# Kernel tuning notes

Measured on AMD Instinct MI355X. Metric: run time of the kernel, lower is better.

Reference implementation:

```python
import jax, jax.numpy as jnp
import numpy as np

EPS = 1e-6

def _l2norm(x):
    # torch F.normalize(dim=1): x / max(||x||_2, eps), norm over channel axis 1
    n = jnp.sqrt(jnp.sum(x * x, axis=1, keepdims=True))
    return x / jnp.maximum(n, EPS)

def setup_inputs() -> dict:
    key = jax.random.key(0)
    ks = jax.random.split(key, 8)
    B, C, Cenc, dk, dv, H, W = 2, 320, 326, 64, 64, 64, 64
    return {
        "x": jax.random.normal(ks[0], (B, C, H, W), jnp.float32),
        "x_enc": jax.random.normal(ks[1], (B, Cenc, H, W), jnp.float32),
        "Wq": jax.random.normal(ks[2], (dk, Cenc), jnp.float32) * 0.05,
        "bq": jnp.zeros((dk,), jnp.float32),
        "Wk": jax.random.normal(ks[3], (dk, Cenc), jnp.float32) * 0.05,
        "bk": jnp.zeros((dk,), jnp.float32),
        "Wv": jax.random.normal(ks[4], (dv, C), jnp.float32) * 0.05,
        "bv": jnp.zeros((dv,), jnp.float32),
    }

def reference(x, x_enc, Wq, bq, Wk, bk, Wv, bv):
    B, C, H, Wd = x.shape
    L = H * Wd
    xe = x_enc.reshape(B, x_enc.shape[1], L)   # [B, Cenc, L]
    xf = x.reshape(B, C, L)                    # [B, C, L]
    # 1x1 conv projections == channel matmuls
    Q = jnp.einsum('oc,bcl->bol', Wq, xe) + bq[None, :, None]  # [B, dk, L]
    K = jnp.einsum('oc,bcl->bol', Wk, xe) + bk[None, :, None]  # [B, dk, L]
    V = jnp.einsum('oc,bcl->bol', Wv, xf) + bv[None, :, None]  # [B, dv, L]
    # cosine (L2-normalized) attention
    Qn = _l2norm(Q)
    Kn = _l2norm(K)
    A = jax.nn.softmax(jnp.einsum('bqi,bqj->bij', Qn, Kn), axis=-1)  # [B, L, L]
    R = jnp.einsum('bij,bvj->bvi', A, V)       # [B, dv, L]
    return R.reshape(B, V.shape[1], H, Wd)
```

## Files before the change

### kernel.cpp

```cpp
#include <hip/hip_runtime.h>


#define L_DIM 4096
#define KPAD 384
#define NSPLIT 8

typedef __attribute__((ext_vector_type(8))) short bf16x8;
typedef __attribute__((ext_vector_type(4))) float f32x4;

__device__ __forceinline__ unsigned short f2bf(float f) {
    unsigned u = __float_as_uint(f);
    u += 0x7fffu + ((u >> 16) & 1u);
    return (unsigned short)(u >> 16);
}

__global__ __launch_bounds__(256) void prep_kernel(
    const float* __restrict__ x, const float* __restrict__ xe,
    const float* __restrict__ Wq, const float* __restrict__ Wk,
    const float* __restrict__ Wv,
    unsigned short* __restrict__ xt_x, unsigned short* __restrict__ xt_xe,
    unsigned short* __restrict__ wbf)
{
    const int z = blockIdx.z;
    if (z == 4) {
        const int bid = blockIdx.y * 64 + blockIdx.x;
        const int idx = bid * 256 + threadIdx.x;
        if (idx >= 3 * 64 * KPAD) return;
        const int t = idx / (64 * KPAD);
        const int rem = idx - t * 64 * KPAD;
        const int d = rem / KPAD, c = rem - d * KPAD;
        const int Cin = (t == 2) ? 320 : 326;
        const float* W = (t == 0) ? Wq : (t == 1 ? Wk : Wv);
        wbf[idx] = (c < Cin) ? f2bf(W[(size_t)d * Cin + c]) : (unsigned short)0;
        return;
    }

    const int src_is_x = z >> 1, b = z & 1;
    const int c0 = blockIdx.y * 64;
    const int l0 = blockIdx.x * 64;
    const int Cin = src_is_x ? 320 : 326;
    const float* src = (src_is_x ? x : xe) + (size_t)b * Cin * L_DIM;
    unsigned short* dst = (src_is_x ? xt_x : xt_xe) + (size_t)b * L_DIM * KPAD;

    __shared__ float tile[64][65];
    const int tid = threadIdx.x;

    for (int it = 0; it < 16; ++it) {
        const int idx = tid + it * 256;
        const int cc = idx >> 6, ll = idx & 63;
        const int c = c0 + cc;
        tile[cc][ll] = (c < Cin) ? src[(size_t)c * L_DIM + l0 + ll] : 0.f;
    }
    __syncthreads();
    for (int it = 0; it < 4; ++it) {
        const int idx = tid + it * 256;
        const int ll = idx >> 4, cq = idx & 15;
        ushort4 o;
        o.x = f2bf(tile[cq * 4 + 0][ll]);
        o.y = f2bf(tile[cq * 4 + 1][ll]);
        o.z = f2bf(tile[cq * 4 + 2][ll]);
        o.w = f2bf(tile[cq * 4 + 3][ll]);
        *(ushort4*)(dst + (size_t)(l0 + ll) * KPAD + c0 + cq * 4) = o;
    }
}

__global__ __launch_bounds__(64) void proj_kernel(
    const unsigned short* __restrict__ xt_xe, const unsigned short* __restrict__ xt_x,
    const unsigned short* __restrict__ wbf,
    const float* __restrict__ bq, const float* __restrict__ bk,
    const float* __restrict__ bv,
    unsigned short* __restrict__ qn, unsigned short* __restrict__ kn,
    unsigned short* __restrict__ vbf)
{
    const int z = blockIdx.y;
    const int tensor = z >> 1, b = z & 1;
    const int l0 = blockIdx.x * 64;
    const int lane = threadIdx.x;
    const int q = lane >> 4, ln = lane & 15;

    const unsigned short* Xt = (tensor == 2 ? xt_x : xt_xe) + (size_t)b * L_DIM * KPAD;
    const unsigned short* W  = wbf + (size_t)tensor * 64 * KPAD;
    const float* bias = (tensor == 0) ? bq : (tensor == 1 ? bk : bv);
    const int ksteps = (tensor == 2) ? 10 : 11;

    f32x4 acc[4][4];
    #pragma unroll
    for (int mf = 0; mf < 4; ++mf)
        #pragma unroll
        for (int nf = 0; nf < 4; ++nf) acc[mf][nf] = (f32x4){0.f, 0.f, 0.f, 0.f};

    bf16x8 af[4], bfr[4], afn[4], bfn[4];
    #pragma unroll
    for (int mf = 0; mf < 4; ++mf)
        af[mf] = *(const bf16x8*)(W + (size_t)(mf * 16 + ln) * KPAD + q * 8);
    #pragma unroll
    for (int nf = 0; nf < 4; ++nf)
        bfr[nf] = *(const bf16x8*)(Xt + (size_t)(l0 + nf * 16 + ln) * KPAD + q * 8);

    for (int ks = 0; ks < ksteps; ++ks) {
        if (ks + 1 < ksteps) {
            const int c = (ks + 1) * 32 + q * 8;
            #pragma unroll
            for (int mf = 0; mf < 4; ++mf)
                afn[mf] = *(const bf16x8*)(W + (size_t)(mf * 16 + ln) * KPAD + c);
            #pragma unroll
            for (int nf = 0; nf < 4; ++nf)
                bfn[nf] = *(const bf16x8*)(Xt + (size_t)(l0 + nf * 16 + ln) * KPAD + c);
        }
        #pragma unroll
        for (int mf = 0; mf < 4; ++mf)
            #pragma unroll
            for (int nf = 0; nf < 4; ++nf)
                acc[mf][nf] = __builtin_amdgcn_mfma_f32_16x16x32_bf16(
                    af[mf], bfr[nf], acc[mf][nf], 0, 0, 0);
        #pragma unroll
        for (int mf = 0; mf < 4; ++mf) af[mf] = afn[mf];
        #pragma unroll
        for (int nf = 0; nf < 4; ++nf) bfr[nf] = bfn[nf];
    }

    #pragma unroll
    for (int mf = 0; mf < 4; ++mf)
        #pragma unroll
        for (int r = 0; r < 4; ++r) {
            const float bb = bias[mf * 16 + q * 4 + r];
            #pragma unroll
            for (int nf = 0; nf < 4; ++nf) acc[mf][nf][r] += bb;
        }

    if (tensor < 2) {
        unsigned short* outp = (tensor ? kn : qn) + (size_t)b * L_DIM * 64;
        #pragma unroll
        for (int nf = 0; nf < 4; ++nf) {
            float s = 0.f;
            #pragma unroll
            for (int mf = 0; mf < 4; ++mf)
                #pragma unroll
                for (int r = 0; r < 4; ++r) s += acc[mf][nf][r] * acc[mf][nf][r];
            s += __shfl_xor(s, 16);
            s += __shfl_xor(s, 32);
            const float rn = 1.0f / fmaxf(sqrtf(s), 1e-6f);
            const size_t lrow = (size_t)(l0 + nf * 16 + ln) * 64;
            #pragma unroll
            for (int mf = 0; mf < 4; ++mf) {
                ushort4 o;
                o.x = f2bf(acc[mf][nf][0] * rn);
                o.y = f2bf(acc[mf][nf][1] * rn);
                o.z = f2bf(acc[mf][nf][2] * rn);
                o.w = f2bf(acc[mf][nf][3] * rn);
                *(ushort4*)(outp + lrow + mf * 16 + q * 4) = o;
            }
        }
    } else {
        unsigned short* outp = vbf + (size_t)b * 64 * L_DIM;
        #pragma unroll
        for (int mf = 0; mf < 4; ++mf)
            #pragma unroll
            for (int r = 0; r < 4; ++r) {
                const int v = mf * 16 + q * 4 + r;
                #pragma unroll
                for (int nf = 0; nf < 4; ++nf)
                    outp[(size_t)v * L_DIM + l0 + nf * 16 + ln] = f2bf(acc[mf][nf][r]);
            }
    }
}

__global__ __launch_bounds__(256) void attn_kernel(
    const unsigned short* __restrict__ qn, const unsigned short* __restrict__ kn,
    const unsigned short* __restrict__ vbf,
    float* __restrict__ opart, float* __restrict__ ssum)
{
    const int b = blockIdx.z, split = blockIdx.y;
    const int i0 = blockIdx.x * 128;
    const int tid = threadIdx.x;
    const int w = tid >> 6, lane = tid & 63, q = lane >> 4, ln = lane & 15;

    const unsigned short* Q = qn + (size_t)b * L_DIM * 64;
    const unsigned short* K = kn + (size_t)b * L_DIM * 64;
    const unsigned short* V = vbf + (size_t)b * 64 * L_DIM;

    __shared__ unsigned short Kb[64][72];
    __shared__ unsigned short Vb[64][72];
    __shared__ unsigned short Pl[4][32][72];

    bf16x8 qa[2][2];
    #pragma unroll
    for (int s = 0; s < 2; ++s) {
        const unsigned short* qp = Q + (size_t)(i0 + w * 32 + s * 16 + ln) * 64 + q * 8;
        qa[s][0] = *(const bf16x8*)(qp);
        qa[s][1] = *(const bf16x8*)(qp + 32);
    }

    f32x4 acc[2][4];
    #pragma unroll
    for (int s = 0; s < 2; ++s)
        #pragma unroll
        for (int vf = 0; vf < 4; ++vf) acc[s][vf] = (f32x4){0.f, 0.f, 0.f, 0.f};
    float rowsum[2] = {0.f, 0.f};
    const f32x4 zero = (f32x4){0.f, 0.f, 0.f, 0.f};

    const int jbase = split * (L_DIM / NSPLIT);
    const int JT = L_DIM / (NSPLIT * 64);

    bf16x8 kst[2], vst[2];
    #pragma unroll
    for (int p = 0; p < 2; ++p) {
        const int idx = p * 256 + tid;
        kst[p] = *(const bf16x8*)(K + (size_t)jbase * 64 + idx * 8);
        vst[p] = *(const bf16x8*)(V + (size_t)(idx >> 3) * L_DIM + jbase + (idx & 7) * 8);
    }
    #pragma unroll
    for (int p = 0; p < 2; ++p) {
        const int idx = p * 256 + tid;
        *(bf16x8*)&Kb[idx >> 3][(idx & 7) * 8] = kst[p];
        *(bf16x8*)&Vb[idx >> 3][(idx & 7) * 8] = vst[p];
    }
    __syncthreads();

    for (int jt = 0; jt < JT; ++jt) {
        if (jt + 1 < JT) {
            const int j0 = jbase + (jt + 1) * 64;
            #pragma unroll
            for (int p = 0; p < 2; ++p) {
                const int idx = p * 256 + tid;
                kst[p] = *(const bf16x8*)(K + (size_t)j0 * 64 + idx * 8);
                vst[p] = *(const bf16x8*)(V + (size_t)(idx >> 3) * L_DIM + j0 + (idx & 7) * 8);
            }
        }

        bf16x8 kf[4][2];
        #pragma unroll
        for (int jf = 0; jf < 4; ++jf) {
            kf[jf][0] = *(const bf16x8*)&Kb[jf * 16 + ln][q * 8];
            kf[jf][1] = *(const bf16x8*)&Kb[jf * 16 + ln][q * 8 + 32];
        }

        #pragma unroll
        for (int s = 0; s < 2; ++s) {
            #pragma unroll
            for (int jf = 0; jf < 4; ++jf) {
                f32x4 st;
                st = __builtin_amdgcn_mfma_f32_16x16x32_bf16(kf[jf][0], qa[s][0], zero, 0, 0, 0);
                st = __builtin_amdgcn_mfma_f32_16x16x32_bf16(kf[jf][1], qa[s][1], st, 0, 0, 0);
                const float p0 = __expf(st[0]);
                const float p1 = __expf(st[1]);
                const float p2 = __expf(st[2]);
                const float p3 = __expf(st[3]);
                rowsum[s] += (p0 + p1) + (p2 + p3);
                ushort4 pk;
                pk.x = f2bf(p0); pk.y = f2bf(p1); pk.z = f2bf(p2); pk.w = f2bf(p3);
                *(ushort4*)&Pl[w][s * 16 + ln][jf * 16 + q * 4] = pk;
            }
        }

        bf16x8 vfr[4][2];
        #pragma unroll
        for (int vf = 0; vf < 4; ++vf) {
            vfr[vf][0] = *(const bf16x8*)&Vb[vf * 16 + ln][q * 8];
            vfr[vf][1] = *(const bf16x8*)&Vb[vf * 16 + ln][q * 8 + 32];
        }

        #pragma unroll
        for (int s = 0; s < 2; ++s) {
            const bf16x8 pb0 = *(const bf16x8*)&Pl[w][s * 16 + ln][q * 8];
            const bf16x8 pb1 = *(const bf16x8*)&Pl[w][s * 16 + ln][q * 8 + 32];
            #pragma unroll
            for (int vf = 0; vf < 4; ++vf) {
                acc[s][vf] = __builtin_amdgcn_mfma_f32_16x16x32_bf16(vfr[vf][0], pb0, acc[s][vf], 0, 0, 0);
                acc[s][vf] = __builtin_amdgcn_mfma_f32_16x16x32_bf16(vfr[vf][1], pb1, acc[s][vf], 0, 0, 0);
            }
        }

        __syncthreads();
        if (jt + 1 < JT) {
            #pragma unroll
            for (int p = 0; p < 2; ++p) {
                const int idx = p * 256 + tid;
                *(bf16x8*)&Kb[idx >> 3][(idx & 7) * 8] = kst[p];
                *(bf16x8*)&Vb[idx >> 3][(idx & 7) * 8] = vst[p];
            }
            __syncthreads();
        }
    }

    #pragma unroll
    for (int s = 0; s < 2; ++s) {
        rowsum[s] += __shfl_xor(rowsum[s], 16);
        rowsum[s] += __shfl_xor(rowsum[s], 32);
    }

    float* Op = opart + ((size_t)(b * NSPLIT + split) * L_DIM + i0 + w * 32) * 64;
    #pragma unroll
    for (int s = 0; s < 2; ++s)
        #pragma unroll
        for (int vf = 0; vf < 4; ++vf) {
            float4 o;
            o.x = acc[s][vf][0]; o.y = acc[s][vf][1];
            o.z = acc[s][vf][2]; o.w = acc[s][vf][3];
            *(float4*)&Op[(s * 16 + ln) * 64 + vf * 16 + q * 4] = o;
        }

    if (q == 0) {
        #pragma unroll
        for (int s = 0; s < 2; ++s)
            ssum[(size_t)(b * NSPLIT + split) * L_DIM + i0 + w * 32 + s * 16 + ln]
                = rowsum[s];
    }
}

__global__ __launch_bounds__(256) void combine_kernel(
    const float* __restrict__ opart, const float* __restrict__ ssum,
    float* __restrict__ out)
{
    const int b = blockIdx.y;
    const int i0 = blockIdx.x * 64;
    const int tid = threadIdx.x;
    __shared__ float t[64][65];
    __shared__ float sinv[64];

    if (tid < 64) {
        float s = 0.f;
        for (int sp = 0; sp < NSPLIT; ++sp)
            s += ssum[(size_t)(b * NSPLIT + sp) * L_DIM + i0 + tid];
        sinv[tid] = 1.0f / s;
    }
    __syncthreads();
    for (int idx = tid; idx < 4096; idx += 256) {
        const int i = idx >> 6, v = idx & 63;
        float a = 0.f;
        for (int sp = 0; sp < NSPLIT; ++sp)
            a += opart[((size_t)(b * NSPLIT + sp) * L_DIM + i0 + i) * 64 + v];
        t[i][v] = a;
    }
    __syncthreads();
    for (int idx = tid; idx < 4096; idx += 256) {
        const int v = idx >> 6, i = idx & 63;
        out[((size_t)(b * 64 + v)) * L_DIM + i0 + i] = t[i][v] * sinv[i];
    }
}

extern "C" void kernel_launch(void* const* d_in, const int* in_sizes, int n_in,
                              void* d_out, int out_size, void* d_ws, size_t ws_size,
                              hipStream_t stream)
{
    const float* x  = (const float*)d_in[0];
    const float* xe = (const float*)d_in[1];
    const float* Wq = (const float*)d_in[2];
    const float* bq = (const float*)d_in[3];
    const float* Wk = (const float*)d_in[4];
    const float* bk = (const float*)d_in[5];
    const float* Wv = (const float*)d_in[6];
    const float* bv = (const float*)d_in[7];
    float* out = (float*)d_out;

    char* ws = (char*)d_ws;
    unsigned short* qn   = (unsigned short*)(ws);
    unsigned short* kn   = (unsigned short*)(ws + (1u << 20));
    unsigned short* vbf  = (unsigned short*)(ws + (2u << 20));
    float*          ss   = (float*)(ws + (3u << 20));
    unsigned short* wb   = (unsigned short*)(ws + (3u << 20) + (512u << 10));
    unsigned short* xtxe = (unsigned short*)(ws + (4u << 20));
    unsigned short* xtx  = (unsigned short*)(ws + (10u << 20));
    float*          op   = (float*)(ws + (8u << 20));

    prep_kernel<<<dim3(64, 6, 5), 256, 0, stream>>>(x, xe, Wq, Wk, Wv, xtx, xtxe, wb);
    proj_kernel<<<dim3(64, 6), 64, 0, stream>>>(xtxe, xtx, wb, bq, bk, bv, qn, kn, vbf);
    attn_kernel<<<dim3(32, NSPLIT, 2), 256, 0, stream>>>(qn, kn, vbf, op, ss);
    combine_kernel<<<dim3(64, 2), 256, 0, stream>>>(op, ss, out);
}
```

Before: 128.4 us.

## Vectorize prep loads, split projection K across two waves, store partials in bf16

The prep kernel now reads the input with float4 loads instead of scalar loads. The projection kernel runs two waves per block, each covering half of the padded channel range, and adds the two partial accumulators through shared memory; this doubles parallelism in a launch of only 384 blocks. Attention partial outputs are stored as bf16 instead of fp32, which halves combine traffic at some precision cost. The combine kernel reads these partials with vectorized ushort4 loads, and the partial buffer moves to a new workspace offset.

```diff
diff --git a/kernel.cpp b/kernel.cpp
--- a/kernel.cpp
+++ b/kernel.cpp
@@ -12,6 +12,10 @@
     unsigned u = __float_as_uint(f);
     u += 0x7fffu + ((u >> 16) & 1u);
     return (unsigned short)(u >> 16);
+}
+
+__device__ __forceinline__ float bf2f(unsigned short h) {
+    return __uint_as_float((unsigned)h << 16);
 }
 
 __global__ __launch_bounds__(256) void prep_kernel(
@@ -45,13 +49,20 @@
     __shared__ float tile[64][65];
     const int tid = threadIdx.x;
 
-    for (int it = 0; it < 16; ++it) {
+    #pragma unroll
+    for (int it = 0; it < 4; ++it) {
         const int idx = tid + it * 256;
-        const int cc = idx >> 6, ll = idx & 63;
+        const int cc = idx >> 4, lq = idx & 15;
         const int c = c0 + cc;
-        tile[cc][ll] = (c < Cin) ? src[(size_t)c * L_DIM + l0 + ll] : 0.f;
+        float4 v = make_float4(0.f, 0.f, 0.f, 0.f);
+        if (c < Cin) v = *(const float4*)(src + (size_t)c * L_DIM + l0 + lq * 4);
+        tile[cc][lq * 4 + 0] = v.x;
+        tile[cc][lq * 4 + 1] = v.y;
+        tile[cc][lq * 4 + 2] = v.z;
+        tile[cc][lq * 4 + 3] = v.w;
     }
     __syncthreads();
+    #pragma unroll
     for (int it = 0; it < 4; ++it) {
         const int idx = tid + it * 256;
         const int ll = idx >> 4, cq = idx & 15;
@@ -64,7 +75,7 @@
     }
 }
 
-__global__ __launch_bounds__(64) void proj_kernel(
+__global__ __launch_bounds__(128) void proj_kernel(
     const unsigned short* __restrict__ xt_xe, const unsigned short* __restrict__ xt_x,
     const unsigned short* __restrict__ wbf,
     const float* __restrict__ bq, const float* __restrict__ bk,
@@ -75,13 +86,15 @@
     const int z = blockIdx.y;
     const int tensor = z >> 1, b = z & 1;
     const int l0 = blockIdx.x * 64;
-    const int lane = threadIdx.x;
+    const int tid = threadIdx.x;
+    const int w = tid >> 6, lane = tid & 63;
     const int q = lane >> 4, ln = lane & 15;
 
     const unsigned short* Xt = (tensor == 2 ? xt_x : xt_xe) + (size_t)b * L_DIM * KPAD;
     const unsigned short* W  = wbf + (size_t)tensor * 64 * KPAD;
     const float* bias = (tensor == 0) ? bq : (tensor == 1 ? bk : bv);
-    const int ksteps = (tensor == 2) ? 10 : 11;
+
+    __shared__ float red[64][68];
 
     f32x4 acc[4][4];
     #pragma unroll
@@ -89,17 +102,19 @@
         #pragma unroll
         for (int nf = 0; nf < 4; ++nf) acc[mf][nf] = (f32x4){0.f, 0.f, 0.f, 0.f};
 
+    const int kbase = w * 6 * 32;
+
     bf16x8 af[4], bfr[4], afn[4], bfn[4];
     #pragma unroll
     for (int mf = 0; mf < 4; ++mf)
-        af[mf] = *(const bf16x8*)(W + (size_t)(mf * 16 + ln) * KPAD + q * 8);
+        af[mf] = *(const bf16x8*)(W + (size_t)(mf * 16 + ln) * KPAD + kbase + q * 8);
     #pragma unroll
     for (int nf = 0; nf < 4; ++nf)
-        bfr[nf] = *(const bf16x8*)(Xt + (size_t)(l0 + nf * 16 + ln) * KPAD + q * 8);
-
-    for (int ks = 0; ks < ksteps; ++ks) {
-        if (ks + 1 < ksteps) {
-            const int c = (ks + 1) * 32 + q * 8;
+        bfr[nf] = *(const bf16x8*)(Xt + (size_t)(l0 + nf * 16 + ln) * KPAD + kbase + q * 8);
+
+    for (int ks = 0; ks < 6; ++ks) {
+        if (ks + 1 < 6) {
+            const int c = kbase + (ks + 1) * 32 + q * 8;
             #pragma unroll
             for (int mf = 0; mf < 4; ++mf)
                 afn[mf] = *(const bf16x8*)(W + (size_t)(mf * 16 + ln) * KPAD + c);
@@ -118,6 +133,24 @@
         #pragma unroll
         for (int nf = 0; nf < 4; ++nf) bfr[nf] = bfn[nf];
     }
+
+    if (w == 1) {
+        #pragma unroll
+        for (int mf = 0; mf < 4; ++mf)
+            #pragma unroll
+            for (int nf = 0; nf < 4; ++nf)
+                *(f32x4*)&red[lane][(mf * 4 + nf) * 4] = acc[mf][nf];
+    }
+    __syncthreads();
+    if (w != 0) return;
+
+    #pragma unroll
+    for (int mf = 0; mf < 4; ++mf)
+        #pragma unroll
+        for (int nf = 0; nf < 4; ++nf) {
+            const f32x4 p = *(const f32x4*)&red[lane][(mf * 4 + nf) * 4];
+            acc[mf][nf] += p;
+        }
 
     #pragma unroll
     for (int mf = 0; mf < 4; ++mf)
@@ -168,7 +201,7 @@
 __global__ __launch_bounds__(256) void attn_kernel(
     const unsigned short* __restrict__ qn, const unsigned short* __restrict__ kn,
     const unsigned short* __restrict__ vbf,
-    float* __restrict__ opart, float* __restrict__ ssum)
+    unsigned short* __restrict__ opart, float* __restrict__ ssum)
 {
     const int b = blockIdx.z, split = blockIdx.y;
     const int i0 = blockIdx.x * 128;
@@ -289,15 +322,15 @@
         rowsum[s] += __shfl_xor(rowsum[s], 32);
     }
 
-    float* Op = opart + ((size_t)(b * NSPLIT + split) * L_DIM + i0 + w * 32) * 64;
+    unsigned short* Op = opart + ((size_t)(b * NSPLIT + split) * L_DIM + i0 + w * 32) * 64;
     #pragma unroll
     for (int s = 0; s < 2; ++s)
         #pragma unroll
         for (int vf = 0; vf < 4; ++vf) {
-            float4 o;
-            o.x = acc[s][vf][0]; o.y = acc[s][vf][1];
-            o.z = acc[s][vf][2]; o.w = acc[s][vf][3];
-            *(float4*)&Op[(s * 16 + ln) * 64 + vf * 16 + q * 4] = o;
+            ushort4 o;
+            o.x = f2bf(acc[s][vf][0]); o.y = f2bf(acc[s][vf][1]);
+            o.z = f2bf(acc[s][vf][2]); o.w = f2bf(acc[s][vf][3]);
+            *(ushort4*)&Op[(s * 16 + ln) * 64 + vf * 16 + q * 4] = o;
         }
 
     if (q == 0) {
@@ -309,7 +342,7 @@
 }
 
 __global__ __launch_bounds__(256) void combine_kernel(
-    const float* __restrict__ opart, const float* __restrict__ ssum,
+    const unsigned short* __restrict__ opart, const float* __restrict__ ssum,
     float* __restrict__ out)
 {
     const int b = blockIdx.y;
@@ -325,12 +358,19 @@
         sinv[tid] = 1.0f / s;
     }
     __syncthreads();
-    for (int idx = tid; idx < 4096; idx += 256) {
-        const int i = idx >> 6, v = idx & 63;
-        float a = 0.f;
-        for (int sp = 0; sp < NSPLIT; ++sp)
-            a += opart[((size_t)(b * NSPLIT + sp) * L_DIM + i0 + i) * 64 + v];
-        t[i][v] = a;
+    for (int it = 0; it < 4; ++it) {
+        const int idx = tid + it * 256;
+        const int i = idx >> 4, vq = idx & 15;
+        float a0 = 0.f, a1 = 0.f, a2 = 0.f, a3 = 0.f;
+        for (int sp = 0; sp < NSPLIT; ++sp) {
+            const ushort4 p = *(const ushort4*)&opart[
+                (((size_t)(b * NSPLIT + sp) * L_DIM + i0 + i)) * 64 + vq * 4];
+            a0 += bf2f(p.x); a1 += bf2f(p.y); a2 += bf2f(p.z); a3 += bf2f(p.w);
+        }
+        t[i][vq * 4 + 0] = a0;
+        t[i][vq * 4 + 1] = a1;
+        t[i][vq * 4 + 2] = a2;
+        t[i][vq * 4 + 3] = a3;
     }
     __syncthreads();
     for (int idx = tid; idx < 4096; idx += 256) {
@@ -361,10 +401,10 @@
     unsigned short* wb   = (unsigned short*)(ws + (3u << 20) + (512u << 10));
     unsigned short* xtxe = (unsigned short*)(ws + (4u << 20));
     unsigned short* xtx  = (unsigned short*)(ws + (10u << 20));
-    float*          op   = (float*)(ws + (8u << 20));
+    unsigned short* op   = (unsigned short*)(ws + (16u << 20));
 
     prep_kernel<<<dim3(64, 6, 5), 256, 0, stream>>>(x, xe, Wq, Wk, Wv, xtx, xtxe, wb);
-    proj_kernel<<<dim3(64, 6), 64, 0, stream>>>(xtxe, xtx, wb, bq, bk, bv, qn, kn, vbf);
+    proj_kernel<<<dim3(64, 6), 128, 0, stream>>>(xtxe, xtx, wb, bq, bk, bv, qn, kn, vbf);
     attn_kernel<<<dim3(32, NSPLIT, 2), 256, 0, stream>>>(qn, kn, vbf, op, ss);
     combine_kernel<<<dim3(64, 2), 256, 0, stream>>>(op, ss, out);
 }
```

Result: faster. 112.1 us (-12.7%).
